# Performance work log

Measured on AMD Instinct MI355X. Metric: run time of the kernel, lower is better.

The kernel has to match this reference:

```python
import jax, jax.numpy as jnp
import numpy as np

B, R, S, D = 8, 128, 512, 33      # batch, ref (grid), seq_len, input_dim (enc_in*2+1)
E, H = 128, 4                     # embed_time, num_heads
EK = E // H                       # per-head dim
NH = 128                          # nhidden
NEG = -1e9


def setup_inputs() -> dict:
    key = jax.random.key(0)
    ks = jax.random.split(key, 16)
    inp = {
        'query': jax.random.normal(ks[0], (B, R, E), jnp.float32),
        'key':   jax.random.normal(ks[1], (B, S, E), jnp.float32),
        'value': jax.random.normal(ks[2], (B, S, D), jnp.float32),
        'mask':  (jax.random.uniform(ks[3], (B, S, D)) < 0.7).astype(jnp.float32),
        'qt':    jnp.sort(jax.random.uniform(ks[4], (R,), jnp.float32)),
        'tt':    jax.random.uniform(ks[5], (B, S), jnp.float32),
        'stride': 0.1 * jax.random.normal(ks[6], (D,), jnp.float32),
        # learned params (torch Linear layout: W [out, in])
        'Wq': jax.random.normal(ks[7], (E, E), jnp.float32) / np.sqrt(E),
        'bq': jnp.zeros((E,), jnp.float32),
        'Wk': jax.random.normal(ks[8], (E, E), jnp.float32) / np.sqrt(E),
        'bk': jnp.zeros((E,), jnp.float32),
        'Wr': jax.random.normal(ks[9], (D, D), jnp.float32) / np.sqrt(D),
        'br': jnp.zeros((D,), jnp.float32),
        'Wo': jax.random.normal(ks[10], (NH, H * D), jnp.float32) / np.sqrt(H * D),
        'bo': jnp.zeros((NH,), jnp.float32),
    }
    return inp


def reference(query, key, value, mask, qt, tt, stride, Wq, bq, Wk, bk, Wr, br, Wo, bo):
    b, r, _ = query.shape
    s = key.shape[1]
    d = value.shape[-1]
    # stride gate: sigmoid(Linear(D,D)(stride))  -> [D]
    sa = jax.nn.sigmoid(stride @ Wr.T + br)
    # projections, split heads: [B,H,R,EK] / [B,H,S,EK]
    q = (query @ Wq.T + bq).reshape(b, r, H, EK).transpose(0, 2, 1, 3)
    k = (key @ Wk.T + bk).reshape(b, s, H, EK).transpose(0, 2, 1, 3)
    # scores: [B,H,R,S]
    scores = jnp.einsum('bhre,bhse->bhrs', q, k) / np.sqrt(EK)
    # per-query time window mask, vectorized over the 'ref' loop: [B,R,S,D]
    t = tt[:, None, :, None]                      # [B,1,S,1]
    qtb = qt[None, :, None, None]                 # [1,R,1,1]
    win = (t <= qtb + sa) & (t >= qtb - sa)       # [B,R,S,D] (sa broadcasts on D)
    allm = win & (mask[:, None, :, :] != 0)       # [B,R,S,D]
    # broadcast scores over value dim D, mask, softmax over seq axis (dim=-2)
    sc = jnp.where(allm[:, None], scores[..., None], NEG)  # [B,H,R,S,D]
    p = jax.nn.softmax(sc, axis=-2)
    # masked weighted sum over seq: [B,H,R,D]
    x = jnp.einsum('bhrsd,bsd->bhrd', p, value)
    x = x.transpose(0, 2, 1, 3).reshape(b, r, H * d)
    out = x @ Wo.T + bo                           # [B,R,NH]
    return out, sa
```

## Files before the change

kernel.cpp:

```cpp
#include <hip/hip_runtime.h>

#define BB   8
#define RR   128
#define SS   512
#define DD   33
#define EE   128
#define HH   4
#define EKK  32
#define NHH  128
#define HD   (HH*DD)

#define WS_SA   0
#define WS_QP   64
#define WS_KT   (WS_QP  + BB*RR*EE)
#define WS_WOT  (WS_KT  + BB*EE*SS)

#define NB_SA   1
#define NB_QP   (BB*RR/8)
#define NB_KT   (BB*SS/16)
#define NB_WOT  ((HD*NHH + 127)/128)
#define NB_PREP (NB_SA + NB_QP + NB_KT + NB_WOT)

__global__ __launch_bounds__(128) void prep_kernel(
    const float* __restrict__ query, const float* __restrict__ key,
    const float* __restrict__ stridev,
    const float* __restrict__ Wq, const float* __restrict__ bq,
    const float* __restrict__ Wk, const float* __restrict__ bk,
    const float* __restrict__ Wr, const float* __restrict__ brv,
    const float* __restrict__ Wo,
    float* __restrict__ ws, float* __restrict__ out_tail)
{
    __shared__ float rows[16 * EE];
    int blk = blockIdx.x, tid = threadIdx.x;

    if (blk == 0) {
        if (tid < DD) {
            float acc = brv[tid];
#pragma unroll
            for (int j = 0; j < DD; ++j) acc += stridev[j] * Wr[tid * DD + j];
            float sv = 1.0f / (1.0f + __expf(-acc));
            ws[WS_SA + tid] = sv;
            out_tail[tid]   = sv;
        }
        return;
    }
    blk -= NB_SA;

    if (blk < NB_QP) {
        int br0 = blk * 8;
#pragma unroll
        for (int p = 0; p < 8; ++p) rows[p * EE + tid] = query[(br0 + p) * EE + tid];
        __syncthreads();
        float acc[8];
        float bv = bq[tid];
#pragma unroll
        for (int p = 0; p < 8; ++p) acc[p] = bv;
        const float4* W4 = (const float4*)(Wq + tid * EE);
        const float4* R4 = (const float4*)rows;
#pragma unroll
        for (int j = 0; j < EE / 4; ++j) {
            float4 w = W4[j];
#pragma unroll
            for (int p = 0; p < 8; ++p) {
                float4 rv = R4[p * 32 + j];
                acc[p] += w.x * rv.x + w.y * rv.y + w.z * rv.z + w.w * rv.w;
            }
        }
#pragma unroll
        for (int p = 0; p < 8; ++p)
            ws[WS_QP + (br0 + p) * EE + tid] = acc[p];
        return;
    }
    blk -= NB_QP;

    if (blk < NB_KT) {
        int s16 = blk * 16;
#pragma unroll
        for (int p = 0; p < 16; ++p) rows[p * EE + tid] = key[(s16 + p) * EE + tid];
        __syncthreads();
        float acc[16];
        float bv = bk[tid];
#pragma unroll
        for (int p = 0; p < 16; ++p) acc[p] = bv;
        const float4* W4 = (const float4*)(Wk + tid * EE);
        const float4* R4 = (const float4*)rows;
#pragma unroll
        for (int j = 0; j < EE / 4; ++j) {
            float4 w = W4[j];
#pragma unroll
            for (int p = 0; p < 16; ++p) {
                float4 rv = R4[p * 32 + j];
                acc[p] += w.x * rv.x + w.y * rv.y + w.z * rv.z + w.w * rv.w;
            }
        }
        int b = s16 / SS, s0 = s16 % SS;
        float4* dst = (float4*)(ws + WS_KT + (b * EE + tid) * SS + s0);
#pragma unroll
        for (int q4 = 0; q4 < 4; ++q4) {
            float4 v; v.x = acc[q4*4]; v.y = acc[q4*4+1]; v.z = acc[q4*4+2]; v.w = acc[q4*4+3];
            dst[q4] = v;
        }
        return;
    }
    blk -= NB_KT;

    {
        int gid = blk * 128 + tid;
        if (gid < HD * NHH) {
            int n = gid & 127, j = gid >> 7;
            ws[WS_WOT + gid] = Wo[n * HD + j];
        }
    }
}

__global__ __launch_bounds__(512) void fused_kernel(
    const float* __restrict__ qp, const float* __restrict__ kt,
    const float* __restrict__ value, const float* __restrict__ maskp,
    const float* __restrict__ tt, const float* __restrict__ qt,
    const float* __restrict__ sa, const float* __restrict__ wot,
    const float* __restrict__ bo, float* __restrict__ out)
{
    __shared__ float s_q[2][EE];
    __shared__ float s_tt[SS];
    __shared__ float s_sa[DD];
    __shared__ float s_pool[4488];
    __shared__ float s_x[2][HD];
    __shared__ float s_part[4][NHH];

    int blk = blockIdx.x;
    int b  = blk >> 6;
    int r0 = (blk & 63) * 2;
    int tid = threadIdx.x;

    if (tid < 256) s_q[tid >> 7][tid & 127] =
        qp[(b * RR + r0 + (tid >> 7)) * EE + (tid & 127)];
    s_tt[tid] = tt[b * SS + tid];
    if (tid < DD) s_sa[tid] = sa[tid];
    __syncthreads();

    {
        int h = tid >> 7, sq = tid & 127;
        const float* kb = kt + (b * EE + h * EKK) * SS;
        float a0[4] = {0,0,0,0}, a1[4] = {0,0,0,0};
#pragma unroll
        for (int e = 0; e < EKK; ++e) {
            float q0 = s_q[0][h * EKK + e];
            float q1 = s_q[1][h * EKK + e];
            const float* krow = kb + e * SS + sq;
#pragma unroll
            for (int si = 0; si < 4; ++si) {
                float kv = krow[si * 128];
                a0[si] += q0 * kv;
                a1[si] += q1 * kv;
            }
        }
        const float scale = 0.17677669529663687f;
#pragma unroll
        for (int si = 0; si < 4; ++si) {
            int s = sq + 128 * si;
            s_pool[s * 4 + h]            = __expf(a0[si] * scale);
            s_pool[(SS + s) * 4 + h]     = __expf(a1[si] * scale);
        }
    }
    __syncthreads();

    int wv = tid >> 6, lane = tid & 63;
    float ps0[HH] = {0,0,0,0}, ps1[HH] = {0,0,0,0};
    float ws0[HH] = {0,0,0,0}, ws1[HH] = {0,0,0,0};
    float vsum = 0.f;

    if (lane < DD) {
        float qtr0 = qt[r0], qtr1 = qt[r0 + 1];
        float sad = s_sa[lane];
        float lo0 = qtr0 - sad, hi0 = qtr0 + sad;
        float lo1 = qtr1 - sad, hi1 = qtr1 + sad;

        const float* vp = value + (size_t)(b * SS + wv * 64) * DD + lane;
        const float* mp = maskp + (size_t)(b * SS + wv * 64) * DD + lane;

        for (int i4 = 0; i4 < 16; ++i4) {
            float4 t4 = *(const float4*)&s_tt[wv * 64 + i4 * 4];
            float tvs[4] = {t4.x, t4.y, t4.z, t4.w};
#pragma unroll
            for (int u = 0; u < 4; ++u) {
                int i = i4 * 4 + u;
                int s = wv * 64 + i;
                float vv = vp[i * DD];
                float mv = mp[i * DD];
                float tv = tvs[u];
                vsum += vv;
                bool mb = (mv != 0.f);
                bool k0 = mb & (tv >= lo0) & (tv <= hi0);
                bool k1 = mb & (tv >= lo1) & (tv <= hi1);
                float4 e0 = *(const float4*)&s_pool[s * 4];
                float4 e1 = *(const float4*)&s_pool[(SS + s) * 4];
                float ev0[4] = {e0.x, e0.y, e0.z, e0.w};
                float ev1[4] = {e1.x, e1.y, e1.z, e1.w};
#pragma unroll
                for (int h = 0; h < HH; ++h) {
                    float p0 = k0 ? ev0[h] : 0.f;
                    ps0[h] += p0; ws0[h] += p0 * vv;
                    float p1 = k1 ? ev1[h] : 0.f;
                    ps1[h] += p1; ws1[h] += p1 * vv;
                }
            }
        }
    }
    __syncthreads();

    float* s_redp = s_pool;
    float* s_redw = s_pool + 2112;
    float* s_redv = s_pool + 4224;

    if (lane < DD) {
#pragma unroll
        for (int h = 0; h < HH; ++h) {
            s_redp[((wv * 2 + 0) * 4 + h) * DD + lane] = ps0[h];
            s_redp[((wv * 2 + 1) * 4 + h) * DD + lane] = ps1[h];
            s_redw[((wv * 2 + 0) * 4 + h) * DD + lane] = ws0[h];
            s_redw[((wv * 2 + 1) * 4 + h) * DD + lane] = ws1[h];
        }
        s_redv[wv * DD + lane] = vsum;
    }
    __syncthreads();

    if (tid < 2 * HH * DD) {
        int rr  = tid / (HH * DD);
        int rem = tid - rr * (HH * DD);
        int h   = rem / DD;
        int d   = rem - h * DD;
        float p = 0.f, w = 0.f;
#pragma unroll
        for (int k = 0; k < 8; ++k) {
            p += s_redp[((k * 2 + rr) * 4 + h) * DD + d];
            w += s_redw[((k * 2 + rr) * 4 + h) * DD + d];
        }
        float xv;
        if (p > 0.f) xv = w / p;
        else {
            float va = 0.f;
#pragma unroll
            for (int k = 0; k < 8; ++k) va += s_redv[k * DD + d];
            xv = va * (1.0f / SS);
        }
        s_x[rr][h * DD + d] = xv;
    }
    __syncthreads();

    {
        int g2 = tid >> 7;
        int rr = g2 >> 1, jg = g2 & 1;
        int n = tid & 127;
        float acc = 0.f;
#pragma unroll
        for (int j = 0; j < 66; ++j)
            acc += s_x[rr][jg * 66 + j] * wot[(jg * 66 + j) * NHH + n];
        s_part[g2][n] = acc;
    }
    __syncthreads();
    if (tid < 256) {
        int rr = tid >> 7, n = tid & 127;
        out[(b * RR + r0 + rr) * NHH + n] =
            bo[n] + s_part[rr * 2][n] + s_part[rr * 2 + 1][n];
    }
}

extern "C" void kernel_launch(void* const* d_in, const int* in_sizes, int n_in,
                              void* d_out, int out_size, void* d_ws, size_t ws_size,
                              hipStream_t stream) {
    const float* query   = (const float*)d_in[0];
    const float* key     = (const float*)d_in[1];
    const float* value   = (const float*)d_in[2];
    const float* mask    = (const float*)d_in[3];
    const float* qt      = (const float*)d_in[4];
    const float* tt      = (const float*)d_in[5];
    const float* stridev = (const float*)d_in[6];
    const float* Wq      = (const float*)d_in[7];
    const float* bq      = (const float*)d_in[8];
    const float* Wk      = (const float*)d_in[9];
    const float* bk      = (const float*)d_in[10];
    const float* Wr      = (const float*)d_in[11];
    const float* brv     = (const float*)d_in[12];
    const float* Wo      = (const float*)d_in[13];
    const float* bo      = (const float*)d_in[14];

    float* out = (float*)d_out;
    float* ws  = (float*)d_ws;

    prep_kernel<<<NB_PREP, 128, 0, stream>>>(
        query, key, stridev, Wq, bq, Wk, bk, Wr, brv, Wo,
        ws, out + BB * RR * NHH);
    fused_kernel<<<BB * 64, 512, 0, stream>>>(
        ws + WS_QP, ws + WS_KT, value, mask,
        tt, qt, ws + WS_SA, ws + WS_WOT, bo, out);
}
```

Measured before the change: 40.02 us.

## Rebalance prep blocks, fuse stride gate into main kernel, remap lanes over D

The prep kernel is reorganised into more, smaller 256-thread blocks (8 rows each), and the stride-gate sigmoid moves into every fused block so prep no longer carries that tiny block. In the fused kernel, exp scores are stored head-major and K is read as float4. The weighted-sum loop now uses all 64 lanes: two sequence positions per wave step over d<32, plus a separate shuffle-reduced pass for column 32. This removes the idle lanes of the old lane<33 loop and the work imbalance in prep, at the cost of recomputing the 33x33 gate in every block and more complex reduction code.

```diff
diff --git a/kernel.cpp b/kernel.cpp
--- a/kernel.cpp
+++ b/kernel.cpp
@@ -10,119 +10,108 @@
 #define NHH  128
 #define HD   (HH*DD)
 
-#define WS_SA   0
-#define WS_QP   64
-#define WS_KT   (WS_QP  + BB*RR*EE)
-#define WS_WOT  (WS_KT  + BB*EE*SS)
-
-#define NB_SA   1
-#define NB_QP   (BB*RR/8)
-#define NB_KT   (BB*SS/16)
-#define NB_WOT  ((HD*NHH + 127)/128)
-#define NB_PREP (NB_SA + NB_QP + NB_KT + NB_WOT)
-
-__global__ __launch_bounds__(128) void prep_kernel(
+#define WS_QP   0
+#define WS_KT   (BB*RR*EE)
+#define WS_WOT  (WS_KT + BB*EE*SS)
+
+#define NB_KP   512
+#define NB_QP2  128
+#define NB_WOT2 66
+#define NB_PREP (NB_KP + NB_QP2 + NB_WOT2)
+
+__global__ __launch_bounds__(256) void prep_kernel(
     const float* __restrict__ query, const float* __restrict__ key,
-    const float* __restrict__ stridev,
     const float* __restrict__ Wq, const float* __restrict__ bq,
     const float* __restrict__ Wk, const float* __restrict__ bk,
-    const float* __restrict__ Wr, const float* __restrict__ brv,
-    const float* __restrict__ Wo,
-    float* __restrict__ ws, float* __restrict__ out_tail)
+    const float* __restrict__ Wo, float* __restrict__ ws)
 {
-    __shared__ float rows[16 * EE];
+    __shared__ float rows[8 * EE];
     int blk = blockIdx.x, tid = threadIdx.x;
 
-    if (blk == 0) {
-        if (tid < DD) {
-            float acc = brv[tid];
-#pragma unroll
-            for (int j = 0; j < DD; ++j) acc += stridev[j] * Wr[tid * DD + j];
-            float sv = 1.0f / (1.0f + __expf(-acc));
-            ws[WS_SA + tid] = sv;
-            out_tail[tid]   = sv;
-        }
-        return;
-    }
-    blk -= NB_SA;
-
-    if (blk < NB_QP) {
-        int br0 = blk * 8;
-#pragma unroll
-        for (int p = 0; p < 8; ++p) rows[p * EE + tid] = query[(br0 + p) * EE + tid];
+    if (blk < NB_KP) {
+        int s8 = blk * 8;
+#pragma unroll
+        for (int i = 0; i < 4; ++i) rows[i * 256 + tid] = key[s8 * EE + i * 256 + tid];
         __syncthreads();
-        float acc[8];
-        float bv = bq[tid];
-#pragma unroll
-        for (int p = 0; p < 8; ++p) acc[p] = bv;
-        const float4* W4 = (const float4*)(Wq + tid * EE);
+        int g = tid >> 7, e = tid & 127;
+        float acc[4];
+        float bv = bk[e];
+#pragma unroll
+        for (int p = 0; p < 4; ++p) acc[p] = bv;
+        const float4* W4 = (const float4*)(Wk + e * EE);
         const float4* R4 = (const float4*)rows;
 #pragma unroll
         for (int j = 0; j < EE / 4; ++j) {
             float4 w = W4[j];
 #pragma unroll
-            for (int p = 0; p < 8; ++p) {
-                float4 rv = R4[p * 32 + j];
+            for (int p = 0; p < 4; ++p) {
+                float4 rv = R4[(g * 4 + p) * 32 + j];
                 acc[p] += w.x * rv.x + w.y * rv.y + w.z * rv.z + w.w * rv.w;
             }
         }
-#pragma unroll
-        for (int p = 0; p < 8; ++p)
-            ws[WS_QP + (br0 + p) * EE + tid] = acc[p];
+        int b = s8 / SS, s0 = s8 % SS;
+        float4 v; v.x = acc[0]; v.y = acc[1]; v.z = acc[2]; v.w = acc[3];
+        *(float4*)(ws + WS_KT + (b * EE + e) * SS + s0 + g * 4) = v;
         return;
     }
-    blk -= NB_QP;
-
-    if (blk < NB_KT) {
-        int s16 = blk * 16;
-#pragma unroll
-        for (int p = 0; p < 16; ++p) rows[p * EE + tid] = key[(s16 + p) * EE + tid];
+    blk -= NB_KP;
+
+    if (blk < NB_QP2) {
+        int br0 = blk * 8;
+#pragma unroll
+        for (int i = 0; i < 4; ++i) rows[i * 256 + tid] = query[br0 * EE + i * 256 + tid];
         __syncthreads();
-        float acc[16];
-        float bv = bk[tid];
-#pragma unroll
-        for (int p = 0; p < 16; ++p) acc[p] = bv;
-        const float4* W4 = (const float4*)(Wk + tid * EE);
+        int g = tid >> 7, e = tid & 127;
+        float acc[4];
+        float bv = bq[e];
+#pragma unroll
+        for (int p = 0; p < 4; ++p) acc[p] = bv;
+        const float4* W4 = (const float4*)(Wq + e * EE);
         const float4* R4 = (const float4*)rows;
 #pragma unroll
         for (int j = 0; j < EE / 4; ++j) {
             float4 w = W4[j];
 #pragma unroll
-            for (int p = 0; p < 16; ++p) {
-                float4 rv = R4[p * 32 + j];
+            for (int p = 0; p < 4; ++p) {
+                float4 rv = R4[(g * 4 + p) * 32 + j];
                 acc[p] += w.x * rv.x + w.y * rv.y + w.z * rv.z + w.w * rv.w;
             }
         }
-        int b = s16 / SS, s0 = s16 % SS;
-        float4* dst = (float4*)(ws + WS_KT + (b * EE + tid) * SS + s0);
-#pragma unroll
-        for (int q4 = 0; q4 < 4; ++q4) {
-            float4 v; v.x = acc[q4*4]; v.y = acc[q4*4+1]; v.z = acc[q4*4+2]; v.w = acc[q4*4+3];
-            dst[q4] = v;
-        }
+#pragma unroll
+        for (int p = 0; p < 4; ++p)
+            ws[WS_QP + (br0 + g * 4 + p) * EE + e] = acc[p];
         return;
     }
-    blk -= NB_KT;
-
-    {
-        int gid = blk * 128 + tid;
+    blk -= NB_QP2;
+
+    {
+        int gid = blk * 256 + tid;
         if (gid < HD * NHH) {
             int n = gid & 127, j = gid >> 7;
             ws[WS_WOT + gid] = Wo[n * HD + j];
         }
     }
 }
+
+#define POOL_REDP 0
+#define POOL_REDW 2048
+#define POOL_REDV 4096
+#define POOL_R32P 4352
+#define POOL_R32W 4416
+#define POOL_R32V 4480
+#define EIDX(rr,h,s) (((rr)*HH+(h))*SS + (s))
 
 __global__ __launch_bounds__(512) void fused_kernel(
     const float* __restrict__ qp, const float* __restrict__ kt,
     const float* __restrict__ value, const float* __restrict__ maskp,
     const float* __restrict__ tt, const float* __restrict__ qt,
-    const float* __restrict__ sa, const float* __restrict__ wot,
+    const float* __restrict__ stridev, const float* __restrict__ Wr,
+    const float* __restrict__ brv, const float* __restrict__ wot,
     const float* __restrict__ bo, float* __restrict__ out)
 {
     __shared__ float s_q[2][EE];
     __shared__ float s_tt[SS];
-    __shared__ float s_sa[DD];
+    __shared__ float s_sa[DD + 3];
     __shared__ float s_pool[4488];
     __shared__ float s_x[2][HD];
     __shared__ float s_part[4][NHH];
@@ -135,115 +124,158 @@
     if (tid < 256) s_q[tid >> 7][tid & 127] =
         qp[(b * RR + r0 + (tid >> 7)) * EE + (tid & 127)];
     s_tt[tid] = tt[b * SS + tid];
-    if (tid < DD) s_sa[tid] = sa[tid];
+    if (tid < DD) {
+        float acc = brv[tid];
+#pragma unroll
+        for (int j = 0; j < DD; ++j) acc += stridev[j] * Wr[tid * DD + j];
+        float sv = 1.0f / (1.0f + __expf(-acc));
+        s_sa[tid] = sv;
+        if (blk == 0) out[BB * RR * NHH + tid] = sv;
+    }
     __syncthreads();
 
     {
         int h = tid >> 7, sq = tid & 127;
         const float* kb = kt + (b * EE + h * EKK) * SS;
-        float a0[4] = {0,0,0,0}, a1[4] = {0,0,0,0};
+        float4 a0 = {0,0,0,0}, a1 = {0,0,0,0};
 #pragma unroll
         for (int e = 0; e < EKK; ++e) {
+            float4 kv = ((const float4*)(kb + e * SS))[sq];
             float q0 = s_q[0][h * EKK + e];
             float q1 = s_q[1][h * EKK + e];
-            const float* krow = kb + e * SS + sq;
-#pragma unroll
-            for (int si = 0; si < 4; ++si) {
-                float kv = krow[si * 128];
-                a0[si] += q0 * kv;
-                a1[si] += q1 * kv;
-            }
+            a0.x += q0 * kv.x; a0.y += q0 * kv.y; a0.z += q0 * kv.z; a0.w += q0 * kv.w;
+            a1.x += q1 * kv.x; a1.y += q1 * kv.y; a1.z += q1 * kv.z; a1.w += q1 * kv.w;
         }
         const float scale = 0.17677669529663687f;
-#pragma unroll
-        for (int si = 0; si < 4; ++si) {
-            int s = sq + 128 * si;
-            s_pool[s * 4 + h]            = __expf(a0[si] * scale);
-            s_pool[(SS + s) * 4 + h]     = __expf(a1[si] * scale);
-        }
+        float4 e0, e1;
+        e0.x = __expf(a0.x * scale); e0.y = __expf(a0.y * scale);
+        e0.z = __expf(a0.z * scale); e0.w = __expf(a0.w * scale);
+        e1.x = __expf(a1.x * scale); e1.y = __expf(a1.y * scale);
+        e1.z = __expf(a1.z * scale); e1.w = __expf(a1.w * scale);
+        ((float4*)&s_pool[EIDX(0, h, 0)])[sq] = e0;
+        ((float4*)&s_pool[EIDX(1, h, 0)])[sq] = e1;
     }
     __syncthreads();
 
     int wv = tid >> 6, lane = tid & 63;
+    int sp = lane >> 5, d = lane & 31;
+    int s0 = wv * 64;
+    float qtr0 = qt[r0], qtr1 = qt[r0 + 1];
+
     float ps0[HH] = {0,0,0,0}, ps1[HH] = {0,0,0,0};
-    float ws0[HH] = {0,0,0,0}, ws1[HH] = {0,0,0,0};
+    float ws0_[HH] = {0,0,0,0}, ws1_[HH] = {0,0,0,0};
     float vsum = 0.f;
-
-    if (lane < DD) {
-        float qtr0 = qt[r0], qtr1 = qt[r0 + 1];
-        float sad = s_sa[lane];
+    {
+        float sad = s_sa[d];
         float lo0 = qtr0 - sad, hi0 = qtr0 + sad;
         float lo1 = qtr1 - sad, hi1 = qtr1 + sad;
-
-        const float* vp = value + (size_t)(b * SS + wv * 64) * DD + lane;
-        const float* mp = maskp + (size_t)(b * SS + wv * 64) * DD + lane;
-
-        for (int i4 = 0; i4 < 16; ++i4) {
-            float4 t4 = *(const float4*)&s_tt[wv * 64 + i4 * 4];
-            float tvs[4] = {t4.x, t4.y, t4.z, t4.w};
-#pragma unroll
-            for (int u = 0; u < 4; ++u) {
-                int i = i4 * 4 + u;
-                int s = wv * 64 + i;
-                float vv = vp[i * DD];
-                float mv = mp[i * DD];
-                float tv = tvs[u];
-                vsum += vv;
-                bool mb = (mv != 0.f);
-                bool k0 = mb & (tv >= lo0) & (tv <= hi0);
-                bool k1 = mb & (tv >= lo1) & (tv <= hi1);
-                float4 e0 = *(const float4*)&s_pool[s * 4];
-                float4 e1 = *(const float4*)&s_pool[(SS + s) * 4];
-                float ev0[4] = {e0.x, e0.y, e0.z, e0.w};
-                float ev1[4] = {e1.x, e1.y, e1.z, e1.w};
-#pragma unroll
-                for (int h = 0; h < HH; ++h) {
-                    float p0 = k0 ? ev0[h] : 0.f;
-                    ps0[h] += p0; ws0[h] += p0 * vv;
-                    float p1 = k1 ? ev1[h] : 0.f;
-                    ps1[h] += p1; ws1[h] += p1 * vv;
-                }
+        const float* vp = value + (size_t)(b * SS + s0 + sp) * DD + d;
+        const float* mp = maskp + (size_t)(b * SS + s0 + sp) * DD + d;
+#pragma unroll 4
+        for (int i = 0; i < 32; ++i) {
+            int s = s0 + 2 * i + sp;
+            float vv = vp[i * 2 * DD];
+            float mv = mp[i * 2 * DD];
+            float tv = s_tt[s];
+            bool mb = (mv != 0.f);
+            bool k0 = mb & (tv >= lo0) & (tv <= hi0);
+            bool k1 = mb & (tv >= lo1) & (tv <= hi1);
+            vsum += vv;
+#pragma unroll
+            for (int h = 0; h < HH; ++h) {
+                float e0 = s_pool[EIDX(0, h, s)];
+                float e1 = s_pool[EIDX(1, h, s)];
+                float p0 = k0 ? e0 : 0.f;
+                float p1 = k1 ? e1 : 0.f;
+                ps0[h] += p0; ws0_[h] += p0 * vv;
+                ps1[h] += p1; ws1_[h] += p1 * vv;
             }
         }
-    }
-    __syncthreads();
-
-    float* s_redp = s_pool;
-    float* s_redw = s_pool + 2112;
-    float* s_redv = s_pool + 4224;
-
-    if (lane < DD) {
 #pragma unroll
         for (int h = 0; h < HH; ++h) {
-            s_redp[((wv * 2 + 0) * 4 + h) * DD + lane] = ps0[h];
-            s_redp[((wv * 2 + 1) * 4 + h) * DD + lane] = ps1[h];
-            s_redw[((wv * 2 + 0) * 4 + h) * DD + lane] = ws0[h];
-            s_redw[((wv * 2 + 1) * 4 + h) * DD + lane] = ws1[h];
-        }
-        s_redv[wv * DD + lane] = vsum;
-    }
-    __syncthreads();
-
-    if (tid < 2 * HH * DD) {
-        int rr  = tid / (HH * DD);
-        int rem = tid - rr * (HH * DD);
-        int h   = rem / DD;
-        int d   = rem - h * DD;
+            ps0[h] += __shfl_xor(ps0[h], 32); ws0_[h] += __shfl_xor(ws0_[h], 32);
+            ps1[h] += __shfl_xor(ps1[h], 32); ws1_[h] += __shfl_xor(ws1_[h], 32);
+        }
+        vsum += __shfl_xor(vsum, 32);
+    }
+
+    float tps = 0.f, tws = 0.f, tvs = 0.f;
+    {
+        int trr = lane >> 5, th = (lane >> 3) & 3, tj = lane & 7;
+        float sad = s_sa[32];
+        float lo = (trr ? qtr1 : qtr0) - sad, hi = (trr ? qtr1 : qtr0) + sad;
+#pragma unroll
+        for (int i = 0; i < 8; ++i) {
+            int s = s0 + tj * 8 + i;
+            float vv = value[(size_t)(b * SS + s) * DD + 32];
+            float mv = maskp[(size_t)(b * SS + s) * DD + 32];
+            float tv = s_tt[s];
+            bool k = (mv != 0.f) & (tv >= lo) & (tv <= hi);
+            float e = s_pool[EIDX(trr, th, s)];
+            float p = k ? e : 0.f;
+            tps += p; tws += p * vv; tvs += vv;
+        }
+#pragma unroll
+        for (int off = 1; off < 8; off <<= 1) {
+            tps += __shfl_xor(tps, off);
+            tws += __shfl_xor(tws, off);
+            tvs += __shfl_xor(tvs, off);
+        }
+    }
+    __syncthreads();
+
+    if (lane < 32) {
+#pragma unroll
+        for (int h = 0; h < HH; ++h) {
+            s_pool[POOL_REDP + ((wv * 2 + 0) * HH + h) * 32 + lane] = ps0[h];
+            s_pool[POOL_REDP + ((wv * 2 + 1) * HH + h) * 32 + lane] = ps1[h];
+            s_pool[POOL_REDW + ((wv * 2 + 0) * HH + h) * 32 + lane] = ws0_[h];
+            s_pool[POOL_REDW + ((wv * 2 + 1) * HH + h) * 32 + lane] = ws1_[h];
+        }
+        s_pool[POOL_REDV + wv * 32 + lane] = vsum;
+    }
+    if ((lane & 7) == 0) {
+        int trr = lane >> 5, th = (lane >> 3) & 3;
+        s_pool[POOL_R32P + (wv * 2 + trr) * HH + th] = tps;
+        s_pool[POOL_R32W + (wv * 2 + trr) * HH + th] = tws;
+        if (lane == 0) s_pool[POOL_R32V + wv] = tvs;
+    }
+    __syncthreads();
+
+    if (tid < 256) {
+        int rr = tid >> 7, hd = tid & 127, h = hd >> 5, dd = hd & 31;
         float p = 0.f, w = 0.f;
 #pragma unroll
         for (int k = 0; k < 8; ++k) {
-            p += s_redp[((k * 2 + rr) * 4 + h) * DD + d];
-            w += s_redw[((k * 2 + rr) * 4 + h) * DD + d];
+            p += s_pool[POOL_REDP + ((k * 2 + rr) * HH + h) * 32 + dd];
+            w += s_pool[POOL_REDW + ((k * 2 + rr) * HH + h) * 32 + dd];
         }
         float xv;
         if (p > 0.f) xv = w / p;
         else {
             float va = 0.f;
 #pragma unroll
-            for (int k = 0; k < 8; ++k) va += s_redv[k * DD + d];
+            for (int k = 0; k < 8; ++k) va += s_pool[POOL_REDV + k * 32 + dd];
             xv = va * (1.0f / SS);
         }
-        s_x[rr][h * DD + d] = xv;
+        s_x[rr][h * DD + dd] = xv;
+    } else if (tid < 264) {
+        int t = tid - 256, rr = t >> 2, h = t & 3;
+        float p = 0.f, w = 0.f;
+#pragma unroll
+        for (int k = 0; k < 8; ++k) {
+            p += s_pool[POOL_R32P + (k * 2 + rr) * HH + h];
+            w += s_pool[POOL_R32W + (k * 2 + rr) * HH + h];
+        }
+        float xv;
+        if (p > 0.f) xv = w / p;
+        else {
+            float va = 0.f;
+#pragma unroll
+            for (int k = 0; k < 8; ++k) va += s_pool[POOL_R32V + k];
+            xv = va * (1.0f / SS);
+        }
+        s_x[rr][h * DD + 32] = xv;
     }
     __syncthreads();
 
@@ -287,10 +319,9 @@
     float* out = (float*)d_out;
     float* ws  = (float*)d_ws;
 
-    prep_kernel<<<NB_PREP, 128, 0, stream>>>(
-        query, key, stridev, Wq, bq, Wk, bk, Wr, brv, Wo,
-        ws, out + BB * RR * NHH);
+    prep_kernel<<<NB_PREP, 256, 0, stream>>>(
+        query, key, Wq, bq, Wk, bk, Wo, ws);
     fused_kernel<<<BB * 64, 512, 0, stream>>>(
-        ws + WS_QP, ws + WS_KT, value, mask,
-        tt, qt, ws + WS_SA, ws + WS_WOT, bo, out);
+        ws + WS_QP, ws + WS_KT, value, mask, tt, qt,
+        stridev, Wr, brv, ws + WS_WOT, bo, out);
 }
```

Result: no change. 39.89 us (-0.3%).
